# Kernel optimization log

Hardware: AMD Instinct MI355X
Metric: run time of the kernel (lower is better)

## Reference

```python
import jax, jax.numpy as jnp
import numpy as np

NUM_CLASSES = 10
LAMBDA_COORD = 5.0
LAMBDA_NOOBJ = 0.5
B, S, P = 2048, 26, 5 + NUM_CLASSES


def setup_inputs() -> dict:
    key = jax.random.key(0)
    k1, k2 = jax.random.split(key)
    predictions = jax.random.normal(k1, (B, S, S, P), dtype=jnp.float32)
    targets = jax.random.normal(k2, (B, S * S * P,), dtype=jnp.float32)
    return {"predictions": predictions, "targets": targets}


def reference(predictions, targets):
    b, s, _, p = predictions.shape
    pred = predictions.reshape(b, s * s, p)          # (B, S*S, 5+C)
    tgt = targets.reshape(b, s * s, -1)              # (B, S*S, 5+C)

    obj = tgt[..., 4] > 0                            # object mask per cell

    # Coordinate loss: lambda_coord * sum((pred_xywh - tgt_xywh)^2) over object cells
    coord_sq = jnp.sum((pred[..., :4] - tgt[..., :4]) ** 2, axis=-1)
    coord_loss = LAMBDA_COORD * jnp.sum(jnp.where(obj, coord_sq, 0.0))

    # Confidence loss: (sigmoid(p_conf) - t_conf)^2 on obj cells,
    # lambda_noobj * sigmoid(p_conf)^2 on no-obj cells (scalar MSE mean == squared diff)
    conf_p = jax.nn.sigmoid(pred[..., 4])
    conf_loss = jnp.sum(jnp.where(obj,
                                  (conf_p - tgt[..., 4]) ** 2,
                                  LAMBDA_NOOBJ * conf_p ** 2))

    # Classification loss: mean over C of squared diff per object cell, summed
    cls_sq = jnp.mean((pred[..., 5:5 + NUM_CLASSES] - tgt[..., 5:5 + NUM_CLASSES]) ** 2, axis=-1)
    class_loss = jnp.sum(jnp.where(obj, cls_sq, 0.0))

    total_loss = coord_loss + conf_loss + class_loss
    return (total_loss, coord_loss, conf_loss, class_loss)
```

## Files before the change

kernel.cpp:

```cpp
#include <hip/hip_runtime.h>

constexpr int   NUM_CLASSES  = 10;
constexpr float LAMBDA_COORD = 5.0f;
constexpr float LAMBDA_NOOBJ = 0.5f;
constexpr int   BLOCK = 256;
constexpr int   NBLOCKS_MAX = 2048;

__global__ __launch_bounds__(BLOCK) void yolo_main(
    const float4* __restrict__ pred4,
    const float4* __restrict__ tgt4,
    const float*  __restrict__ tgt,
    float* __restrict__ ws,
    unsigned n4, unsigned nblocks)
{
    unsigned idx    = blockIdx.x * BLOCK + threadIdx.x;
    unsigned stride = nblocks * BLOCK;

    float coord = 0.f, conf = 0.f, cls = 0.f;

    for (unsigned k = idx; k < n4; k += stride) {
        float4 p = pred4[k];
        float4 t = tgt4[k];
        unsigned base  = 4u * k;
        unsigned cell0 = base / 15u;
        unsigned j0    = base - cell0 * 15u;

        float t4a = tgt[cell0 * 15u + 4u];
        float t4b = (j0 >= 12u) ? tgt[cell0 * 15u + 19u] : t4a;

        float pm[4] = {p.x, p.y, p.z, p.w};
        float tm[4] = {t.x, t.y, t.z, t.w};

#pragma unroll
        for (int m = 0; m < 4; ++m) {
            unsigned j      = j0 + (unsigned)m;
            bool     second = j >= 15u;
            unsigned jj     = second ? j - 15u : j;
            float    t4     = second ? t4b : t4a;
            bool     obj    = t4 > 0.f;

            float d  = pm[m] - tm[m];
            float sq = d * d;

            float sig   = 1.f / (1.f + __expf(-pm[m]));
            float dsv   = sig - tm[m];
            float confv = obj ? dsv * dsv : LAMBDA_NOOBJ * sig * sig;

            if (jj < 4u)       { if (obj) coord += sq; }
            else if (jj == 4u) { conf += confv; }
            else               { if (obj) cls += sq; }
        }
    }

#pragma unroll
    for (int off = 32; off > 0; off >>= 1) {
        coord += __shfl_down(coord, off);
        conf  += __shfl_down(conf,  off);
        cls   += __shfl_down(cls,   off);
    }

    __shared__ float s[3][4];
    int wave = threadIdx.x >> 6, lane = threadIdx.x & 63;
    if (lane == 0) { s[0][wave] = coord; s[1][wave] = conf; s[2][wave] = cls; }
    __syncthreads();

    if (threadIdx.x == 0) {
        float c0 = s[0][0] + s[0][1] + s[0][2] + s[0][3];
        float c1 = s[1][0] + s[1][1] + s[1][2] + s[1][3];
        float c2 = s[2][0] + s[2][1] + s[2][2] + s[2][3];
        ws[blockIdx.x]               = c0;
        ws[nblocks + blockIdx.x]     = c1;
        ws[2 * nblocks + blockIdx.x] = c2;
    }
}

__global__ __launch_bounds__(BLOCK) void yolo_finalize(
    const float* __restrict__ ws, float* __restrict__ out, unsigned nblocks)
{
    float c0 = 0.f, c1 = 0.f, c2 = 0.f;
    for (unsigned i = threadIdx.x; i < nblocks; i += BLOCK) {
        c0 += ws[i];
        c1 += ws[nblocks + i];
        c2 += ws[2 * nblocks + i];
    }
#pragma unroll
    for (int off = 32; off > 0; off >>= 1) {
        c0 += __shfl_down(c0, off);
        c1 += __shfl_down(c1, off);
        c2 += __shfl_down(c2, off);
    }
    __shared__ float s[3][4];
    int wave = threadIdx.x >> 6, lane = threadIdx.x & 63;
    if (lane == 0) { s[0][wave] = c0; s[1][wave] = c1; s[2][wave] = c2; }
    __syncthreads();
    if (threadIdx.x == 0) {
        float coord = LAMBDA_COORD * (s[0][0] + s[0][1] + s[0][2] + s[0][3]);
        float conf  =                 s[1][0] + s[1][1] + s[1][2] + s[1][3];
        float cls   = (1.f / NUM_CLASSES) * (s[2][0] + s[2][1] + s[2][2] + s[2][3]);
        out[0] = coord + conf + cls;
        out[1] = coord;
        out[2] = conf;
        out[3] = cls;
    }
}

extern "C" void kernel_launch(void* const* d_in, const int* in_sizes, int n_in,
                              void* d_out, int out_size, void* d_ws, size_t ws_size,
                              hipStream_t stream) {
    const float* pred = (const float*)d_in[0];
    const float* tgt  = (const float*)d_in[1];
    float* out = (float*)d_out;
    float* ws  = (float*)d_ws;

    unsigned total = (unsigned)in_sizes[0];
    unsigned n4    = total / 4u;

    unsigned nblocks = NBLOCKS_MAX;
    size_t need = (size_t)nblocks * 3 * sizeof(float);
    if (need > ws_size) nblocks = (unsigned)(ws_size / (3 * sizeof(float)));

    yolo_main<<<nblocks, BLOCK, 0, stream>>>(
        (const float4*)pred, (const float4*)tgt, tgt, ws, n4, nblocks);
    yolo_finalize<<<1, BLOCK, 0, stream>>>(ws, out, nblocks);
}
```

Before: 182.9 us.

## Tile cells per block and stage objectness flags in shared memory

Each block now handles tiles of 256 cells (960 float4s) and keeps 8 float4 loads per thread in flight. Each cell's objectness target is written to a shared-memory array, replacing the scattered per-element global re-reads of tgt[cell*15+4]. The sigmoid is now computed only for the confidence element, not for every element, which removes most exp and reciprocal work and switches to a hardware rcp. The cost is two block barriers per tile, more register use, and a tile count that assumes the cell count divides by 256; any leftover cells would be silently ignored.

```diff
diff --git a/kernel.cpp b/kernel.cpp
--- a/kernel.cpp
+++ b/kernel.cpp
@@ -4,51 +4,92 @@
 constexpr float LAMBDA_COORD = 5.0f;
 constexpr float LAMBDA_NOOBJ = 0.5f;
 constexpr int   BLOCK = 256;
-constexpr int   NBLOCKS_MAX = 2048;
+constexpr int   CELLS_PER_TILE = 256;
+constexpr int   F4_PER_TILE    = 960;
+constexpr int   NBLOCKS_MAX    = 2048;
 
 __global__ __launch_bounds__(BLOCK) void yolo_main(
     const float4* __restrict__ pred4,
     const float4* __restrict__ tgt4,
-    const float*  __restrict__ tgt,
     float* __restrict__ ws,
-    unsigned n4, unsigned nblocks)
+    unsigned ntiles, unsigned nblocks)
 {
-    unsigned idx    = blockIdx.x * BLOCK + threadIdx.x;
-    unsigned stride = nblocks * BLOCK;
+    __shared__ float flag[CELLS_PER_TILE + 1];
+
+    const unsigned tid  = threadIdx.x;
+    const bool     has3 = tid < (unsigned)(F4_PER_TILE - 768);
 
     float coord = 0.f, conf = 0.f, cls = 0.f;
 
-    for (unsigned k = idx; k < n4; k += stride) {
-        float4 p = pred4[k];
-        float4 t = tgt4[k];
-        unsigned base  = 4u * k;
-        unsigned cell0 = base / 15u;
-        unsigned j0    = base - cell0 * 15u;
+    for (unsigned tile = blockIdx.x; tile < ntiles; tile += nblocks) {
+        const unsigned tb = tile * F4_PER_TILE;
 
-        float t4a = tgt[cell0 * 15u + 4u];
-        float t4b = (j0 >= 12u) ? tgt[cell0 * 15u + 19u] : t4a;
+        float4 t[4], p[4];
+        t[0] = tgt4[tb + tid];
+        t[1] = tgt4[tb + tid + 256u];
+        t[2] = tgt4[tb + tid + 512u];
+        t[3] = has3 ? tgt4[tb + tid + 768u] : float4{0.f, 0.f, 0.f, 0.f};
+        p[0] = pred4[tb + tid];
+        p[1] = pred4[tb + tid + 256u];
+        p[2] = pred4[tb + tid + 512u];
+        p[3] = has3 ? pred4[tb + tid + 768u] : float4{0.f, 0.f, 0.f, 0.f};
 
-        float pm[4] = {p.x, p.y, p.z, p.w};
-        float tm[4] = {t.x, t.y, t.z, t.w};
+        __syncthreads();
 
 #pragma unroll
-        for (int m = 0; m < 4; ++m) {
-            unsigned j      = j0 + (unsigned)m;
-            bool     second = j >= 15u;
-            unsigned jj     = second ? j - 15u : j;
-            float    t4     = second ? t4b : t4a;
-            bool     obj    = t4 > 0.f;
+        for (int q = 0; q < 4; ++q) {
+            if (q == 3 && !has3) continue;
+            unsigned lb    = 4u * (tid + 256u * (unsigned)q);
+            unsigned lcell = lb / 15u;
+            unsigned j0    = lb - lcell * 15u;
+            float tm[4] = {t[q].x, t[q].y, t[q].z, t[q].w};
+#pragma unroll
+            for (int m = 0; m < 4; ++m) {
+                unsigned j   = j0 + (unsigned)m;
+                bool     sec = j >= 15u;
+                unsigned jj  = sec ? j - 15u : j;
+                if (jj == 4u) flag[lcell + (sec ? 1u : 0u)] = tm[m];
+            }
+        }
+        __syncthreads();
 
-            float d  = pm[m] - tm[m];
-            float sq = d * d;
+#pragma unroll
+        for (int q = 0; q < 4; ++q) {
+            if (q == 3 && !has3) continue;
+            unsigned lb    = 4u * (tid + 256u * (unsigned)q);
+            unsigned lcell = lb / 15u;
+            unsigned j0    = lb - lcell * 15u;
+            float t4a = flag[lcell];
+            float t4b = flag[lcell + 1u];
+            float pm[4] = {p[q].x, p[q].y, p[q].z, p[q].w};
+            float tm[4] = {t[q].x, t[q].y, t[q].z, t[q].w};
 
-            float sig   = 1.f / (1.f + __expf(-pm[m]));
-            float dsv   = sig - tm[m];
-            float confv = obj ? dsv * dsv : LAMBDA_NOOBJ * sig * sig;
+            float pc = 0.f, tc = 0.f;
+            bool  hasc = false;
 
-            if (jj < 4u)       { if (obj) coord += sq; }
-            else if (jj == 4u) { conf += confv; }
-            else               { if (obj) cls += sq; }
+#pragma unroll
+            for (int m = 0; m < 4; ++m) {
+                unsigned j   = j0 + (unsigned)m;
+                bool     sec = j >= 15u;
+                unsigned jj  = sec ? j - 15u : j;
+                float    t4  = sec ? t4b : t4a;
+                bool     obj = t4 > 0.f;
+
+                float d  = pm[m] - tm[m];
+                float sq = d * d;
+
+                if (jj == 4u) { pc = pm[m]; tc = tm[m]; hasc = true; }
+                else if (obj) {
+                    if (jj < 4u) coord += sq;
+                    else         cls   += sq;
+                }
+            }
+            if (hasc) {
+                float e   = __expf(-pc);
+                float sig = __builtin_amdgcn_rcpf(1.f + e);
+                float ds  = sig - tc;
+                conf += (tc > 0.f) ? ds * ds : LAMBDA_NOOBJ * sig * sig;
+            }
         }
     }
 
@@ -65,12 +106,9 @@
     __syncthreads();
 
     if (threadIdx.x == 0) {
-        float c0 = s[0][0] + s[0][1] + s[0][2] + s[0][3];
-        float c1 = s[1][0] + s[1][1] + s[1][2] + s[1][3];
-        float c2 = s[2][0] + s[2][1] + s[2][2] + s[2][3];
-        ws[blockIdx.x]               = c0;
-        ws[nblocks + blockIdx.x]     = c1;
-        ws[2 * nblocks + blockIdx.x] = c2;
+        ws[blockIdx.x]               = s[0][0] + s[0][1] + s[0][2] + s[0][3];
+        ws[nblocks + blockIdx.x]     = s[1][0] + s[1][1] + s[1][2] + s[1][3];
+        ws[2 * nblocks + blockIdx.x] = s[2][0] + s[2][1] + s[2][2] + s[2][3];
     }
 }
 
@@ -112,14 +150,16 @@
     float* out = (float*)d_out;
     float* ws  = (float*)d_ws;
 
-    unsigned total = (unsigned)in_sizes[0];
-    unsigned n4    = total / 4u;
+    unsigned total  = (unsigned)in_sizes[0];
+    unsigned ncells = total / 15u;
+    unsigned ntiles = ncells / CELLS_PER_TILE;
 
     unsigned nblocks = NBLOCKS_MAX;
-    size_t need = (size_t)nblocks * 3 * sizeof(float);
-    if (need > ws_size) nblocks = (unsigned)(ws_size / (3 * sizeof(float)));
+    if ((size_t)nblocks * 3 * sizeof(float) > ws_size)
+        nblocks = (unsigned)(ws_size / (3 * sizeof(float)));
+    if (nblocks > ntiles) nblocks = ntiles;
 
     yolo_main<<<nblocks, BLOCK, 0, stream>>>(
-        (const float4*)pred, (const float4*)tgt, tgt, ws, n4, nblocks);
+        (const float4*)pred, (const float4*)tgt, ws, ntiles, nblocks);
     yolo_finalize<<<1, BLOCK, 0, stream>>>(ws, out, nblocks);
 }
```

Result: no change. 184.8 us (+1.1%).
